# Kernel tuning notes

Hardware: AMD Instinct MI355X
Metric: run time of the kernel (lower is better)

Reference implementation:

```python
import jax, jax.numpy as jnp
import numpy as np

ENC_DIM, DEC_DIM, ATT_DIM = 512, 512, 512
B, S = 32, 4096


def setup_inputs() -> dict:
    key = jax.random.key(0)
    ks = jax.random.split(key, 8)
    sc = lambda d: 1.0 / np.sqrt(d)
    return {
        "input": jax.random.normal(ks[0], (B, S, ENC_DIM), dtype=jnp.float32),
        "dec_h": jax.random.normal(ks[1], (B, DEC_DIM), dtype=jnp.float32),
        "W_enc": jax.random.uniform(ks[2], (ENC_DIM, ATT_DIM), jnp.float32, -sc(ENC_DIM), sc(ENC_DIM)),
        "b_enc": jax.random.uniform(ks[3], (ATT_DIM,), jnp.float32, -sc(ENC_DIM), sc(ENC_DIM)),
        "W_dec": jax.random.uniform(ks[4], (DEC_DIM, ATT_DIM), jnp.float32, -sc(DEC_DIM), sc(DEC_DIM)),
        "b_dec": jax.random.uniform(ks[5], (ATT_DIM,), jnp.float32, -sc(DEC_DIM), sc(DEC_DIM)),
        "w_att": jax.random.uniform(ks[6], (ATT_DIM, 1), jnp.float32, -sc(ATT_DIM), sc(ATT_DIM)),
        "b_att": jax.random.uniform(ks[7], (1,), jnp.float32, -sc(ATT_DIM), sc(ATT_DIM)),
    }


def reference(input, dec_h, W_enc, b_enc, W_dec, b_dec, w_att, b_att):
    # enc_att: [B,S,A]; dec_att: [B,A] broadcast over S
    enc_att = jnp.einsum("bse,ea->bsa", input, W_enc) + b_enc
    dec_att = dec_h @ W_dec + b_dec
    # score: [B,S]
    att = jax.nn.relu(enc_att + dec_att[:, None, :]) @ w_att + b_att  # [B,S,1]
    prob = jax.nn.softmax(att, axis=1)  # softmax over sequence dim
    weighted = jnp.sum(input * prob, axis=1)  # [B,enc_dim]
    return weighted, prob[..., 0]
```

## Files before the change

kernel.cpp:

```cpp
#include <hip/hip_runtime.h>
#include <hip/hip_bf16.h>

typedef __attribute__((ext_vector_type(4))) float f32x4;
typedef __attribute__((ext_vector_type(8))) __bf16 bf16x8;
typedef __attribute__((ext_vector_type(4))) unsigned int u32x4;


__device__ __forceinline__ float lo_bf(unsigned int u) {
  return __builtin_bit_cast(float, u << 16);
}
__device__ __forceinline__ float hi_bf(unsigned int u) {
  return __builtin_bit_cast(float, u & 0xffff0000u);
}

__device__ __forceinline__ void barrier_lgkm() {
  asm volatile("s_waitcnt lgkmcnt(0)" ::: "memory");
  __builtin_amdgcn_s_barrier();
  asm volatile("" ::: "memory");
}

__global__ void prep_w(const float* __restrict__ W_enc, unsigned short* __restrict__ Wf) {
  int idx = blockIdx.x * 256 + threadIdx.x;
  int lane = idx & 63;
  int g = idx >> 6;
  int nt = g & 3, kb = (g >> 2) & 15, w = g >> 6;
  int n = (w * 4 + nt) * 16 + (lane & 15);
  int k0 = kb * 32 + (lane >> 4) * 8;
  unsigned short* dst = Wf + idx * 8;
  #pragma unroll
  for (int j = 0; j < 8; ++j) {
    float f = W_enc[(k0 + j) * 512 + n];
    dst[j] = __builtin_bit_cast(unsigned short, (__bf16)f);
  }
}

__global__ void prep_c(const float* __restrict__ dec_h, const float* __restrict__ W_dec,
                       const float* __restrict__ b_dec, const float* __restrict__ b_enc,
                       float* __restrict__ cpart) {
  int b = blockIdx.x >> 2, j = blockIdx.x & 3;
  int a = threadIdx.x;
  const float* dh = dec_h + b * 512 + j * 128;
  const float* wd = W_dec + (j * 128) * 512 + a;
  float s = (j == 0) ? (b_dec[a] + b_enc[a]) : 0.f;
  #pragma unroll 8
  for (int k = 0; k < 128; ++k) s += dh[k] * wd[k * 512];
  cpart[j * 16384 + b * 512 + a] = s;
}

__global__ __launch_bounds__(1024, 4) void attn_main(
    const float* __restrict__ input, const unsigned short* __restrict__ Wf,
    const float* __restrict__ cpart, const float* __restrict__ w_att,
    float* __restrict__ att_out, float* __restrict__ m_out, float* __restrict__ pw_out) {
  __shared__ u32x4 A4[8192];
  __shared__ float c_lds[512];
  __shared__ float w_lds[512];
  __shared__ float red[8][64];
  __shared__ float red2[8 * 8 * 72];

  char* Al = (char*)A4;
  const int tid = threadIdx.x;
  const int wave = tid >> 6, lane = tid & 63;
  const int l15 = lane & 15, l4 = lane >> 4;
  const int blk = blockIdx.x;
  const int ci0 = blk * 8;
  const int b = ci0 >> 6;
  const bool is_stage = wave >= 8;
  const int st_id = tid & 511;

  float4 g[4][2];

  auto STAGE_HALF = [&](int ci, int bufsel, int half) {
    const float* base = input + (long)ci * 32768;
    char* dst = Al + bufsel * 65536;
    #pragma unroll
    for (int j = 0; j < 4; ++j) {
      int ch = st_id + j * 512;
      int row = (ch >> 6) + half * 32, c32 = ch & 63;
      const float4* s4 = (const float4*)(base + row * 512 + c32 * 8);
      g[j][0] = s4[0];
      g[j][1] = s4[1];
    }
    #pragma unroll
    for (int j = 0; j < 4; ++j) {
      int ch = st_id + j * 512;
      int row = (ch >> 6) + half * 32, c32 = ch & 63;
      bf16x8 v;
      v[0] = (__bf16)g[j][0].x; v[1] = (__bf16)g[j][0].y;
      v[2] = (__bf16)g[j][0].z; v[3] = (__bf16)g[j][0].w;
      v[4] = (__bf16)g[j][1].x; v[5] = (__bf16)g[j][1].y;
      v[6] = (__bf16)g[j][1].z; v[7] = (__bf16)g[j][1].w;
      *(bf16x8*)(dst + row * 1024 + ((c32 * 16) ^ ((row & 7) << 4))) = v;
    }
  };

  if (!is_stage) {
    c_lds[tid] = cpart[b * 512 + tid] + cpart[16384 + b * 512 + tid]
               + cpart[32768 + b * 512 + tid] + cpart[49152 + b * 512 + tid];
    w_lds[tid] = w_att[tid];
  } else {
    STAGE_HALF(ci0, 0, 0);
    STAGE_HALF(ci0, 0, 1);
  }
  barrier_lgkm();

  const bf16x8* Wfp = (const bf16x8*)Wf;

  for (int i = 0; i < 8; ++i) {
    const int ci = ci0 + i;
    const char* Ab = Al + (i & 1) * 65536;

    if (!is_stage) {
      f32x4 acc[4][4];
      #pragma unroll
      for (int nt = 0; nt < 4; ++nt)
        #pragma unroll
        for (int st = 0; st < 4; ++st) {
          f32x4 z = {0.f, 0.f, 0.f, 0.f};
          acc[nt][st] = z;
        }
      const bf16x8* wb = Wfp + (wave * 64) * 64 + lane;
      #pragma unroll 2
      for (int kb = 0; kb < 16; ++kb) {
        bf16x8 av4[4];
        #pragma unroll
        for (int nt = 0; nt < 4; ++nt)
          av4[nt] = wb[(kb * 4 + nt) * 64];
        __builtin_amdgcn_s_setprio(1);
        #pragma unroll
        for (int st = 0; st < 4; ++st) {
          int row = st * 16 + l15;
          bf16x8 xf = *(const bf16x8*)(Ab + row * 1024 + (((kb * 64) + l4 * 16) ^ ((row & 7) << 4)));
          #pragma unroll
          for (int nt = 0; nt < 4; ++nt)
            acc[nt][st] = __builtin_amdgcn_mfma_f32_16x16x32_bf16(av4[nt], xf, acc[nt][st], 0, 0, 0);
        }
        __builtin_amdgcn_s_setprio(0);
      }
      float attp[4] = {0.f, 0.f, 0.f, 0.f};
      #pragma unroll
      for (int nt = 0; nt < 4; ++nt) {
        #pragma unroll
        for (int r = 0; r < 4; ++r) {
          int n = (wave * 4 + nt) * 16 + l4 * 4 + r;
          float cc = c_lds[n], ww = w_lds[n];
          #pragma unroll
          for (int st = 0; st < 4; ++st)
            attp[st] += fmaxf(acc[nt][st][r] + cc, 0.f) * ww;
        }
      }
      #pragma unroll
      for (int st = 0; st < 4; ++st) {
        attp[st] += __shfl_xor(attp[st], 16, 64);
        attp[st] += __shfl_xor(attp[st], 32, 64);
      }
      if (l4 == 0) {
        #pragma unroll
        for (int st = 0; st < 4; ++st)
          red[wave][st * 16 + l15] = attp[st];
      }
    } else if (i < 7) {
      STAGE_HALF(ci + 1, (i + 1) & 1, 0);
    }
    barrier_lgkm();

    if (!is_stage) {
      float av = 0.f;
      #pragma unroll
      for (int cw = 0; cw < 8; ++cw) av += red[cw][lane];
      float m = av;
      #pragma unroll
      for (int off = 32; off >= 1; off >>= 1) m = fmaxf(m, __shfl_xor(m, off, 64));
      float p = expf(av - m);
      if (wave == 0) {
        att_out[b * 4096 + (ci & 63) * 64 + lane] = av;
        if (lane == 0) m_out[ci] = m;
      }
      float acc8[8] = {0.f, 0.f, 0.f, 0.f, 0.f, 0.f, 0.f, 0.f};
      #pragma unroll
      for (int j = 0; j < 8; ++j) {
        int s = wave * 8 + j;
        float ps = __shfl(p, s, 64);
        u32x4 u = *(const u32x4*)(Ab + s * 1024 + ((lane * 16) ^ ((s & 7) << 4)));
        acc8[0] += ps * lo_bf(u[0]); acc8[1] += ps * hi_bf(u[0]);
        acc8[2] += ps * lo_bf(u[1]); acc8[3] += ps * hi_bf(u[1]);
        acc8[4] += ps * lo_bf(u[2]); acc8[5] += ps * hi_bf(u[2]);
        acc8[6] += ps * lo_bf(u[3]); acc8[7] += ps * hi_bf(u[3]);
      }
      #pragma unroll
      for (int q = 0; q < 8; ++q)
        red2[(wave * 8 + q) * 72 + lane] = acc8[q];
    } else if (i < 7) {
      STAGE_HALF(ci + 1, (i + 1) & 1, 1);
    }
    barrier_lgkm();

    if (tid < 512) {
      int lw = tid >> 3, q = tid & 7;
      float s = 0.f;
      #pragma unroll
      for (int w = 0; w < 8; ++w) s += red2[(w * 8 + q) * 72 + lw];
      pw_out[ci * 512 + lw * 8 + q] = s;
    }
    barrier_lgkm();
  }
}

__global__ void finalize(const float* __restrict__ att, const float* __restrict__ m_blk,
                         const float* __restrict__ pw, float* __restrict__ out) {
  const int bg = blockIdx.x;
  const int b = bg >> 2, g = bg & 3;
  const int tid = threadIdx.x;
  const int wave = tid >> 6, lane = tid & 63;
  __shared__ float wred[4];
  __shared__ float zred[4];
  __shared__ float fac[64];

  float v[16];
  float mx = -3.4e38f;
  #pragma unroll
  for (int i = 0; i < 16; ++i) {
    v[i] = att[b * 4096 + i * 256 + tid];
    mx = fmaxf(mx, v[i]);
  }
  #pragma unroll
  for (int off = 32; off >= 1; off >>= 1) mx = fmaxf(mx, __shfl_xor(mx, off, 64));
  if (lane == 0) wred[wave] = mx;
  __syncthreads();
  mx = fmaxf(fmaxf(wred[0], wred[1]), fmaxf(wred[2], wred[3]));

  float z = 0.f;
  #pragma unroll
  for (int i = 0; i < 16; ++i) { v[i] = expf(v[i] - mx); z += v[i]; }
  #pragma unroll
  for (int off = 32; off >= 1; off >>= 1) z += __shfl_xor(z, off, 64);
  if (lane == 0) zred[wave] = z;
  __syncthreads();
  z = zred[0] + zred[1] + zred[2] + zred[3];
  float invZ = 1.f / z;

  #pragma unroll
  for (int i = 0; i < 4; ++i) {
    int ii = g * 4 + i;
    out[16384 + b * 4096 + ii * 256 + tid] = v[ii] * invZ;
  }

  if (tid < 64) fac[tid] = expf(m_blk[b * 64 + tid] - mx) * invZ;
  __syncthreads();

  int col = g * 128 + (tid >> 1);
  int h = tid & 1;
  float w0 = 0.f;
  #pragma unroll 8
  for (int s = h * 32; s < h * 32 + 32; ++s)
    w0 += fac[s] * pw[(b * 64 + s) * 512 + col];
  w0 += __shfl_xor(w0, 1, 64);
  if (h == 0) out[b * 512 + col] = w0;
}

extern "C" void kernel_launch(void* const* d_in, const int* in_sizes, int n_in,
                              void* d_out, int out_size, void* d_ws, size_t ws_size,
                              hipStream_t stream) {
  const float* input = (const float*)d_in[0];
  const float* dec_h = (const float*)d_in[1];
  const float* W_enc = (const float*)d_in[2];
  const float* b_enc = (const float*)d_in[3];
  const float* W_dec = (const float*)d_in[4];
  const float* b_dec = (const float*)d_in[5];
  const float* w_att = (const float*)d_in[6];
  float* out = (float*)d_out;

  char* ws = (char*)d_ws;
  unsigned short* Wf = (unsigned short*)(ws);
  float* cpart = (float*)(ws + 524288);
  float* att   = (float*)(ws + 786432);
  float* m_b   = (float*)(ws + 1310720);
  float* pw    = (float*)(ws + 1318912);

  hipLaunchKernelGGL(prep_w, dim3(128), dim3(256), 0, stream, W_enc, Wf);
  hipLaunchKernelGGL(prep_c, dim3(128), dim3(512), 0, stream, dec_h, W_dec, b_dec, b_enc, cpart);
  hipLaunchKernelGGL(attn_main, dim3(256), dim3(1024), 0, stream, input, Wf, cpart, w_att, att, m_b, pw);
  hipLaunchKernelGGL(finalize, dim3(128), dim3(256), 0, stream, att, m_b, pw, out);
}
```

Measured before the change: 113.9 us.

## Drop warp-specialized staging for single-buffered 512-thread blocks with more blocks

The change removes the producer/consumer split, where 8 waves staged the next chunk while 8 waves ran MFMA into double-buffered LDS. Blocks become 512 threads, with each thread loading and converting its own chunk into a single LDS buffer. Each block handles 4 chunks instead of 8, and the grid grows to 512 blocks. The weighted-sum step now reduces within the wave using shuffles and drops the red2 LDS reduction and one barrier. This halves LDS use per block to allow more resident blocks for latency hiding, at the cost of losing the explicit overlap of global loads with compute inside a block.

```diff
diff --git a/kernel.cpp b/kernel.cpp
--- a/kernel.cpp
+++ b/kernel.cpp
@@ -47,69 +47,62 @@
   cpart[j * 16384 + b * 512 + a] = s;
 }
 
-__global__ __launch_bounds__(1024, 4) void attn_main(
+__global__ __launch_bounds__(512, 4) void attn_main(
     const float* __restrict__ input, const unsigned short* __restrict__ Wf,
     const float* __restrict__ cpart, const float* __restrict__ w_att,
     float* __restrict__ att_out, float* __restrict__ m_out, float* __restrict__ pw_out) {
-  __shared__ u32x4 A4[8192];
+  __shared__ u32x4 A4[4096];
   __shared__ float c_lds[512];
   __shared__ float w_lds[512];
   __shared__ float red[8][64];
-  __shared__ float red2[8 * 8 * 72];
 
   char* Al = (char*)A4;
   const int tid = threadIdx.x;
   const int wave = tid >> 6, lane = tid & 63;
   const int l15 = lane & 15, l4 = lane >> 4;
   const int blk = blockIdx.x;
-  const int ci0 = blk * 8;
+  const int ci0 = blk * 4;
   const int b = ci0 >> 6;
-  const bool is_stage = wave >= 8;
-  const int st_id = tid & 511;
-
-  float4 g[4][2];
-
-  auto STAGE_HALF = [&](int ci, int bufsel, int half) {
-    const float* base = input + (long)ci * 32768;
-    char* dst = Al + bufsel * 65536;
-    #pragma unroll
-    for (int j = 0; j < 4; ++j) {
-      int ch = st_id + j * 512;
-      int row = (ch >> 6) + half * 32, c32 = ch & 63;
-      const float4* s4 = (const float4*)(base + row * 512 + c32 * 8);
-      g[j][0] = s4[0];
-      g[j][1] = s4[1];
+
+  c_lds[tid] = cpart[b * 512 + tid] + cpart[16384 + b * 512 + tid]
+             + cpart[32768 + b * 512 + tid] + cpart[49152 + b * 512 + tid];
+  w_lds[tid] = w_att[tid];
+
+  const bf16x8* Wfp = (const bf16x8*)Wf;
+  const bf16x8* wb = Wfp + (wave * 64) * 64 + lane;
+
+  for (int i = 0; i < 4; ++i) {
+    const int ci = ci0 + i;
+
+    {
+      const float* base = input + (long)ci * 32768;
+      #pragma unroll
+      for (int half = 0; half < 2; ++half) {
+        float4 g[4][2];
+        #pragma unroll
+        for (int j = 0; j < 4; ++j) {
+          int ch = tid + (half * 4 + j) * 512;
+          int row = ch >> 6, c32 = ch & 63;
+          const float4* s4 = (const float4*)(base + row * 512 + c32 * 8);
+          g[j][0] = s4[0];
+          g[j][1] = s4[1];
+        }
+        #pragma unroll
+        for (int j = 0; j < 4; ++j) {
+          int ch = tid + (half * 4 + j) * 512;
+          int row = ch >> 6, c32 = ch & 63;
+          bf16x8 v;
+          v[0] = (__bf16)g[j][0].x; v[1] = (__bf16)g[j][0].y;
+          v[2] = (__bf16)g[j][0].z; v[3] = (__bf16)g[j][0].w;
+          v[4] = (__bf16)g[j][1].x; v[5] = (__bf16)g[j][1].y;
+          v[6] = (__bf16)g[j][1].z; v[7] = (__bf16)g[j][1].w;
+          *(bf16x8*)(Al + row * 1024 + ((c32 * 16) ^ ((row & 7) << 4))) = v;
+        }
+      }
     }
-    #pragma unroll
-    for (int j = 0; j < 4; ++j) {
-      int ch = st_id + j * 512;
-      int row = (ch >> 6) + half * 32, c32 = ch & 63;
-      bf16x8 v;
-      v[0] = (__bf16)g[j][0].x; v[1] = (__bf16)g[j][0].y;
-      v[2] = (__bf16)g[j][0].z; v[3] = (__bf16)g[j][0].w;
-      v[4] = (__bf16)g[j][1].x; v[5] = (__bf16)g[j][1].y;
-      v[6] = (__bf16)g[j][1].z; v[7] = (__bf16)g[j][1].w;
-      *(bf16x8*)(dst + row * 1024 + ((c32 * 16) ^ ((row & 7) << 4))) = v;
-    }
-  };
-
-  if (!is_stage) {
-    c_lds[tid] = cpart[b * 512 + tid] + cpart[16384 + b * 512 + tid]
-               + cpart[32768 + b * 512 + tid] + cpart[49152 + b * 512 + tid];
-    w_lds[tid] = w_att[tid];
-  } else {
-    STAGE_HALF(ci0, 0, 0);
-    STAGE_HALF(ci0, 0, 1);
-  }
-  barrier_lgkm();
-
-  const bf16x8* Wfp = (const bf16x8*)Wf;
-
-  for (int i = 0; i < 8; ++i) {
-    const int ci = ci0 + i;
-    const char* Ab = Al + (i & 1) * 65536;
-
-    if (!is_stage) {
+    barrier_lgkm();
+
+    {
       f32x4 acc[4][4];
       #pragma unroll
       for (int nt = 0; nt < 4; ++nt)
@@ -118,8 +111,7 @@
           f32x4 z = {0.f, 0.f, 0.f, 0.f};
           acc[nt][st] = z;
         }
-      const bf16x8* wb = Wfp + (wave * 64) * 64 + lane;
-      #pragma unroll 2
+      #pragma unroll
       for (int kb = 0; kb < 16; ++kb) {
         bf16x8 av4[4];
         #pragma unroll
@@ -129,7 +121,7 @@
         #pragma unroll
         for (int st = 0; st < 4; ++st) {
           int row = st * 16 + l15;
-          bf16x8 xf = *(const bf16x8*)(Ab + row * 1024 + (((kb * 64) + l4 * 16) ^ ((row & 7) << 4)));
+          bf16x8 xf = *(const bf16x8*)(Al + row * 1024 + (((kb * 64) + l4 * 16) ^ ((row & 7) << 4)));
           #pragma unroll
           for (int nt = 0; nt < 4; ++nt)
             acc[nt][st] = __builtin_amdgcn_mfma_f32_16x16x32_bf16(av4[nt], xf, acc[nt][st], 0, 0, 0);
@@ -158,12 +150,10 @@
         for (int st = 0; st < 4; ++st)
           red[wave][st * 16 + l15] = attp[st];
       }
-    } else if (i < 7) {
-      STAGE_HALF(ci + 1, (i + 1) & 1, 0);
     }
     barrier_lgkm();
 
-    if (!is_stage) {
+    {
       float av = 0.f;
       #pragma unroll
       for (int cw = 0; cw < 8; ++cw) av += red[cw][lane];
@@ -175,31 +165,24 @@
         att_out[b * 4096 + (ci & 63) * 64 + lane] = av;
         if (lane == 0) m_out[ci] = m;
       }
-      float acc8[8] = {0.f, 0.f, 0.f, 0.f, 0.f, 0.f, 0.f, 0.f};
-      #pragma unroll
-      for (int j = 0; j < 8; ++j) {
-        int s = wave * 8 + j;
+      const int li = lane & 31;
+      const int s0 = (lane >> 5) * 32;
+      const int ub = (wave * 32 + li) * 4;
+      float a0 = 0.f, a1 = 0.f;
+      #pragma unroll 8
+      for (int j = 0; j < 32; ++j) {
+        int s = s0 + j;
         float ps = __shfl(p, s, 64);
-        u32x4 u = *(const u32x4*)(Ab + s * 1024 + ((lane * 16) ^ ((s & 7) << 4)));
-        acc8[0] += ps * lo_bf(u[0]); acc8[1] += ps * hi_bf(u[0]);
-        acc8[2] += ps * lo_bf(u[1]); acc8[3] += ps * hi_bf(u[1]);
-        acc8[4] += ps * lo_bf(u[2]); acc8[5] += ps * hi_bf(u[2]);
-        acc8[6] += ps * lo_bf(u[3]); acc8[7] += ps * hi_bf(u[3]);
-      }
-      #pragma unroll
-      for (int q = 0; q < 8; ++q)
-        red2[(wave * 8 + q) * 72 + lane] = acc8[q];
-    } else if (i < 7) {
-      STAGE_HALF(ci + 1, (i + 1) & 1, 1);
-    }
-    barrier_lgkm();
-
-    if (tid < 512) {
-      int lw = tid >> 3, q = tid & 7;
-      float s = 0.f;
-      #pragma unroll
-      for (int w = 0; w < 8; ++w) s += red2[(w * 8 + q) * 72 + lw];
-      pw_out[ci * 512 + lw * 8 + q] = s;
+        unsigned int u = *(const unsigned int*)(Al + s * 1024 + (ub ^ ((s & 7) << 4)));
+        a0 += ps * lo_bf(u);
+        a1 += ps * hi_bf(u);
+      }
+      a0 += __shfl_xor(a0, 32, 64);
+      a1 += __shfl_xor(a1, 32, 64);
+      if (lane < 32) {
+        pw_out[ci * 512 + wave * 64 + li * 2]     = a0;
+        pw_out[ci * 512 + wave * 64 + li * 2 + 1] = a1;
+      }
     }
     barrier_lgkm();
   }
@@ -278,6 +261,6 @@
 
   hipLaunchKernelGGL(prep_w, dim3(128), dim3(256), 0, stream, W_enc, Wf);
   hipLaunchKernelGGL(prep_c, dim3(128), dim3(512), 0, stream, dec_h, W_dec, b_dec, b_enc, cpart);
-  hipLaunchKernelGGL(attn_main, dim3(256), dim3(1024), 0, stream, input, Wf, cpart, w_att, att, m_b, pw);
+  hipLaunchKernelGGL(attn_main, dim3(512), dim3(512), 0, stream, input, Wf, cpart, w_att, att, m_b, pw);
   hipLaunchKernelGGL(finalize, dim3(128), dim3(256), 0, stream, att, m_b, pw, out);
 }
```

Result: slower. 253.0 us (+122.1%).
